# Kernel optimization log

Hardware: AMD Instinct MI355X
Metric: run time of the kernel (lower is better)

## Reference

```python
import jax, jax.numpy as jnp
import numpy as np

B, LQ, LK = 1, 2048, 2048
D, H, KVH, DH = 4096, 32, 8, 128
G = H // KVH  # head groups


def setup_inputs() -> dict:
    key = jax.random.key(0)
    ks = jax.random.split(key, 7)
    s = 0.02
    hidden_q = jax.random.normal(ks[0], (B, LQ, D), dtype=jnp.float32)
    hidden_kv = jax.random.normal(ks[1], (B, LK, D), dtype=jnp.float32)
    # causal boolean mask (batch, len_q, len_k)
    attention_mask = jnp.broadcast_to(jnp.tril(jnp.ones((LQ, LK), dtype=bool)), (B, LQ, LK))
    position_bias = jax.random.normal(ks[2], (H, LQ, LK), dtype=jnp.float32) * 0.1
    Wq = jax.random.normal(ks[3], (D, H * DH), dtype=jnp.float32) * s
    Wk = jax.random.normal(ks[4], (D, KVH * DH), dtype=jnp.float32) * s
    Wv = jax.random.normal(ks[5], (D, KVH * DH), dtype=jnp.float32) * s
    Wo = jax.random.normal(ks[6], (H * DH, D), dtype=jnp.float32) * s
    return {"hidden_q": hidden_q, "hidden_kv": hidden_kv,
            "attention_mask": attention_mask, "position_bias": position_bias,
            "Wq": Wq, "Wk": Wk, "Wv": Wv, "Wo": Wo}


def reference(hidden_q, hidden_kv, attention_mask, position_bias, Wq, Wk, Wv, Wo):
    inv4 = DH ** -0.25  # q and k each scaled by dim_head**-1/4
    q = (hidden_q @ Wq) * inv4            # [B, LQ, H*DH]
    k = (hidden_kv @ Wk) * inv4           # [B, LK, KVH*DH]
    v = hidden_kv @ Wv                     # [B, LK, KVH*DH]
    q = q.reshape(B, LQ, KVH, G, DH)       # group heads for GQA
    k = k.reshape(B, LK, KVH, DH)
    v = v.reshape(B, LK, KVH, DH)
    # score: [B, KVH, G, LQ, LK] -> [B, H, LQ, LK]
    score = jnp.einsum('bqkgd,blkd->bkgql', q, k).reshape(B, H, LQ, LK)
    score = score + position_bias[None]
    mask = attention_mask[:, None]         # [B, 1, LQ, LK]
    score = jnp.where(mask, score, -jnp.inf)
    p = jax.nn.softmax(score, axis=-1)
    p = jnp.where(mask, p, 0.0)
    out = jnp.einsum('bkgql,blkd->bqkgd', p.reshape(B, KVH, G, LQ, LK), v)
    out = out.reshape(B, LQ, H * DH) @ Wo  # [B, LQ, D]
    return out
```

## Files before the change

### kernel.cpp

```cpp
#include <hip/hip_runtime.h>
#include <hip/hip_bf16.h>
#include <cstdint>
#include <cstddef>

typedef __attribute__((ext_vector_type(4))) float f32x4;
typedef __attribute__((ext_vector_type(4))) short s16x4;
typedef __attribute__((ext_vector_type(8))) short s16x8;

#define SLQ 2048
#define SLK 2048
#define SNH 32
#define SDH 128

__device__ __forceinline__ short f2bf(float x) {
  unsigned u = __builtin_bit_cast(unsigned, x);
  u += 0x7FFF + ((u >> 16) & 1);
  return (short)(u >> 16);
}

__device__ __forceinline__ void gload_lds16(const void* g, const void* l) {
  __builtin_amdgcn_global_load_lds((const __attribute__((address_space(1))) void*)g,
                                   (__attribute__((address_space(3))) void*)l,
                                   16, 0, 0);
}

template<int CTRL>
__device__ __forceinline__ float dpp_f32(float x) {
  return __builtin_bit_cast(float, __builtin_amdgcn_update_dpp(
      0, __builtin_bit_cast(int, x), CTRL, 0xF, 0xF, true));
}
__device__ __forceinline__ float rowmax16(float x) {
  x = fmaxf(x, dpp_f32<0x128>(x));
  x = fmaxf(x, dpp_f32<0x124>(x));
  x = fmaxf(x, dpp_f32<0x122>(x));
  x = fmaxf(x, dpp_f32<0x121>(x));
  return x;
}
__device__ __forceinline__ float rowsum16(float x) {
  x += dpp_f32<0x128>(x);
  x += dpp_f32<0x124>(x);
  x += dpp_f32<0x122>(x);
  x += dpp_f32<0x121>(x);
  return x;
}

__global__ void convert_bf16_2(const float* __restrict__ in0, short* __restrict__ out0,
                               const float* __restrict__ in1, short* __restrict__ out1) {
  const int i = blockIdx.x * 256 + threadIdx.x;
  const float* in = blockIdx.y ? in1 : in0;
  short* out = blockIdx.y ? out1 : out0;
  f32x4 a = ((const f32x4*)in)[i];
  s16x4 b;
  b[0] = f2bf(a[0]); b[1] = f2bf(a[1]); b[2] = f2bf(a[2]); b[3] = f2bf(a[3]);
  ((s16x4*)out)[i] = b;
}

__global__ void transpose_all(const float* __restrict__ Wq, const float* __restrict__ Wo,
                              const float* __restrict__ Wk, const float* __restrict__ Wv,
                              short* __restrict__ WqT, short* __restrict__ WoT,
                              short* __restrict__ WkT, short* __restrict__ WvT) {
  __shared__ short T[64][68];
  const int K = 4096;
  int bx = blockIdx.x;
  const float* W; short* Wt; int N;
  if (bx < 64)       { W = Wq; Wt = WqT; N = 4096; }
  else if (bx < 128) { W = Wo; Wt = WoT; N = 4096; bx -= 64; }
  else if (bx < 144) { W = Wk; Wt = WkT; N = 1024; bx -= 128; }
  else               { W = Wv; Wt = WvT; N = 1024; bx -= 144; }
  const int tid = threadIdx.x;
  const int k0 = blockIdx.y * 64, n0 = bx * 64;
  const int r = tid >> 4;
  const int c4 = (tid & 15) * 4;
#pragma unroll
  for (int i = 0; i < 4; ++i) {
    f32x4 a = *(const f32x4*)(W + (size_t)(k0 + r + i * 16) * N + n0 + c4);
#pragma unroll
    for (int j = 0; j < 4; ++j) T[c4 + j][r + i * 16] = f2bf(a[j]);
  }
  __syncthreads();
  const int rn = tid >> 3;
  const int c8 = (tid & 7) * 8;
#pragma unroll
  for (int i = 0; i < 2; ++i) {
    s16x4 v0 = *(const s16x4*)&T[rn + i * 32][c8];
    s16x4 v1 = *(const s16x4*)&T[rn + i * 32][c8 + 4];
    short* dst = Wt + (size_t)(n0 + rn + i * 32) * K + k0 + c8;
    *(s16x4*)dst = v0;
    *(s16x4*)(dst + 4) = v1;
  }
}

template<int CM>
__global__ __launch_bounds__(512, 1)
void gemm_big(const short* __restrict__ A, const short* __restrict__ Bt,
              void* __restrict__ Cv, float scale) {
  __shared__ short As[3][128 * 64];
  __shared__ short Bs[3][256 * 64];
  const int N = 4096, K = 4096;
  const int tid = threadIdx.x, lane = tid & 63, w = tid >> 6;
  const int l15 = lane & 15, lg = lane >> 4;
  const int wr = w >> 2, wc = w & 3;
  const int nbx = N >> 8;
  const int nwg = gridDim.x, b = blockIdx.x;
  const int wg = (b & 7) * (nwg >> 3) + (b >> 3);
  const int m0 = (wg / nbx) * 128, n0 = (wg % nbx) * 256;

  f32x4 acc[4][4];
#pragma unroll
  for (int a = 0; a < 4; ++a)
#pragma unroll
    for (int c = 0; c < 4; ++c)
      acc[a][c] = (f32x4){0.f, 0.f, 0.f, 0.f};

#define GSTAGE(T, BUF) do {                                                    \
    _Pragma("unroll") for (int i_ = 0; i_ < 2; ++i_) {                         \
      const int ci = i_ * 512 + tid, r_ = ci >> 3, c_ = ci & 7;                \
      gload_lds16(A + (size_t)(m0 + r_) * K + (T) * 64 + ((c_ ^ (r_ & 7)) * 8),\
                  (const short*)As[BUF] + ci * 8); }                           \
    _Pragma("unroll") for (int i_ = 0; i_ < 4; ++i_) {                         \
      const int ci = i_ * 512 + tid, r_ = ci >> 3, c_ = ci & 7;                \
      gload_lds16(Bt + (size_t)(n0 + r_) * K + (T) * 64 + ((c_ ^ (r_ & 7)) * 8),\
                  (const short*)Bs[BUF] + ci * 8); }                           \
  } while (0)

  const int NT = K >> 6;
  GSTAGE(0, 0); GSTAGE(1, 1); GSTAGE(2, 2);
  int buf = 0;
  for (int t = 0; t < NT; ++t) {
    if (t + 2 < NT)      asm volatile("s_waitcnt vmcnt(12)" ::: "memory");
    else if (t + 1 < NT) asm volatile("s_waitcnt vmcnt(6)" ::: "memory");
    else                 asm volatile("s_waitcnt vmcnt(0)" ::: "memory");
    __builtin_amdgcn_s_barrier();
    const short* Ab = As[buf];
    const short* Bb = Bs[buf];
    s16x8 af[2][4], bfv[2][4];
#pragma unroll
    for (int kk = 0; kk < 2; ++kk) {
#pragma unroll
      for (int mi = 0; mi < 4; ++mi) {
        const int r = wr * 64 + mi * 16 + l15;
        const int c = (kk * 4 + lg) ^ (r & 7);
        af[kk][mi] = *(const s16x8*)(Ab + (r * 8 + c) * 8);
      }
#pragma unroll
      for (int ni = 0; ni < 4; ++ni) {
        const int r = wc * 64 + ni * 16 + l15;
        const int c = (kk * 4 + lg) ^ (r & 7);
        bfv[kk][ni] = *(const s16x8*)(Bb + (r * 8 + c) * 8);
      }
    }
    __builtin_amdgcn_s_setprio(1);
#pragma unroll
    for (int kk = 0; kk < 2; ++kk)
#pragma unroll
      for (int mi = 0; mi < 4; ++mi)
#pragma unroll
        for (int ni = 0; ni < 4; ++ni)
          acc[mi][ni] = __builtin_amdgcn_mfma_f32_16x16x32_bf16(af[kk][mi], bfv[kk][ni], acc[mi][ni], 0, 0, 0);
    __builtin_amdgcn_s_setprio(0);
    __builtin_amdgcn_s_barrier();
    if (t + 3 < NT) GSTAGE(t + 3, buf);
    buf = (buf == 2) ? 0 : buf + 1;
  }
#undef GSTAGE
#pragma unroll
  for (int mi = 0; mi < 4; ++mi) {
#pragma unroll
    for (int ni = 0; ni < 4; ++ni) {
#pragma unroll
      for (int j = 0; j < 4; ++j) {
        const int rg = m0 + wr * 64 + mi * 16 + lg * 4 + j;
        const int cg = n0 + wc * 64 + ni * 16 + l15;
        const float vv = acc[mi][ni][j] * scale;
        if (CM == 0) ((short*)Cv)[(size_t)rg * N + cg] = f2bf(vv);
        else         ((float*)Cv)[(size_t)rg * N + cg] = vv;
      }
    }
  }
}

__global__ __launch_bounds__(256, 2)
void gemm_kv(const short* __restrict__ A, const short* __restrict__ Bt,
             short* __restrict__ kout, short* __restrict__ vTout, float inv4) {
  __shared__ short As[128][32];
  __shared__ short Bs[128][32];
  const int N = 2048, K = 4096;
  const int tid = threadIdx.x, lane = tid & 63, wid = tid >> 6;
  const int l15 = lane & 15, lg = lane >> 4;
  const int nbx = N >> 7;
  const int nwg = gridDim.x, b = blockIdx.x;
  const int wg = (b & 7) * (nwg >> 3) + (b >> 3);
  const int m0 = (wg / nbx) * 128, n0 = (wg % nbx) * 128;
  const int wm = (wid >> 1) * 64, wn = (wid & 1) * 64;

  f32x4 acc[4][4];
#pragma unroll
  for (int a = 0; a < 4; ++a)
#pragma unroll
    for (int c = 0; c < 4; ++c)
      acc[a][c] = (f32x4){0.f, 0.f, 0.f, 0.f};

  for (int k0 = 0; k0 < K; k0 += 32) {
#pragma unroll
    for (int i = 0; i < 2; ++i) {
      const int c = i * 256 + wid * 64 + lane;
      const int rr = c >> 2, hh = (c & 3) * 8;
      gload_lds16(A  + (size_t)(m0 + rr) * K + k0 + hh,
                  (const short*)As + (size_t)(i * 256 + wid * 64) * 8);
      gload_lds16(Bt + (size_t)(n0 + rr) * K + k0 + hh,
                  (const short*)Bs + (size_t)(i * 256 + wid * 64) * 8);
    }
    __syncthreads();
    s16x8 af[4], bf[4];
#pragma unroll
    for (int mi = 0; mi < 4; ++mi)
      af[mi] = *(const s16x8*)&As[wm + mi * 16 + l15][lg * 8];
#pragma unroll
    for (int ni = 0; ni < 4; ++ni)
      bf[ni] = *(const s16x8*)&Bs[wn + ni * 16 + l15][lg * 8];
#pragma unroll
    for (int mi = 0; mi < 4; ++mi)
#pragma unroll
      for (int ni = 0; ni < 4; ++ni)
        acc[mi][ni] = __builtin_amdgcn_mfma_f32_16x16x32_bf16(af[mi], bf[ni], acc[mi][ni], 0, 0, 0);
    __syncthreads();
  }
  if (n0 < 1024) {
#pragma unroll
    for (int mi = 0; mi < 4; ++mi)
#pragma unroll
      for (int ni = 0; ni < 4; ++ni)
#pragma unroll
        for (int j = 0; j < 4; ++j) {
          const int rg = m0 + wm + mi * 16 + lg * 4 + j;
          const int cg = n0 + wn + ni * 16 + l15;
          kout[(size_t)rg * 1024 + cg] = f2bf(acc[mi][ni][j] * inv4);
        }
  } else {
#pragma unroll
    for (int mi = 0; mi < 4; ++mi)
#pragma unroll
      for (int ni = 0; ni < 4; ++ni) {
        s16x4 wv;
#pragma unroll
        for (int j = 0; j < 4; ++j) wv[j] = f2bf(acc[mi][ni][j]);
        const int rg0 = m0 + wm + mi * 16 + lg * 4;
        const int cg = n0 + wn + ni * 16 + l15 - 1024;
        *(s16x4*)(vTout + (size_t)cg * 2048 + rg0) = wv;
      }
  }
}

__global__ __launch_bounds__(256, 2)
void attn_kernel(const short* __restrict__ q, const short* __restrict__ k,
                 const short* __restrict__ vT, const float* __restrict__ bias,
                 short* __restrict__ o) {
  __shared__ __align__(16) short Ks[64 * 128];
  __shared__ __align__(16) short Vs[2][128 * 64];
  __shared__ __align__(16) float Bb[64 * 64];
  __shared__ __align__(16) short Ps[4][16][72];
  const int tid = threadIdx.x, lane = tid & 63, w = tid >> 6;
  const int l15 = lane & 15, lg = lane >> 4;
  const int b = blockIdx.x;
  const int h = b & 31;
  const int qt = 31 - (b >> 5);
  const int kvh = h >> 2;
  const int nt = qt + 1;

#define STAGE_K(IT) do { const int kv0_ = (IT) * 64;                          \
    _Pragma("unroll") for (int i_ = 0; i_ < 4; ++i_) {                        \
      const int ci = i_ * 256 + tid, r_ = ci >> 4, c_ = ci & 15;              \
      gload_lds16(k + (size_t)(kv0_ + r_) * 1024 + kvh * 128 + ((c_ ^ (r_ & 7)) * 8), \
                  (const short*)Ks + ci * 8); } } while (0)

#define STAGE_V(IT, P) do { const int kv0_ = (IT) * 64;                       \
    _Pragma("unroll") for (int i_ = 0; i_ < 4; ++i_) {                        \
      const int ci = i_ * 256 + tid, r_ = ci >> 3, c_ = ci & 7;               \
      gload_lds16(vT + (size_t)(kvh * 128 + r_) * 2048 + kv0_ + ((c_ ^ (r_ & 7)) * 8), \
                  (const short*)Vs[P] + ci * 8); } } while (0)

#define STAGE_B(IT) do { const int kv0_ = (IT) * 64;                          \
    _Pragma("unroll") for (int i_ = 0; i_ < 4; ++i_) {                        \
      const int ci = i_ * 256 + tid, r_ = ci >> 4, c_ = ci & 15;              \
      gload_lds16(bias + ((size_t)h * SLQ + qt * 64 + r_) * SLK + kv0_ + ((c_ ^ (r_ & 7)) * 4), \
                  (const float*)Bb + ci * 4); } } while (0)

  const int qrow0 = qt * 64 + w * 16 + lg * 4;

  s16x8 qf[4];
  {
    const short* qp = q + (size_t)(qt * 64 + w * 16 + l15) * (SNH * SDH) + h * SDH + lg * 8;
#pragma unroll
    for (int kk = 0; kk < 4; ++kk) qf[kk] = *(const s16x8*)(qp + kk * 32);
  }
  float mrow[4], lrow[4];
  f32x4 oacc[8];
#pragma unroll
  for (int j = 0; j < 4; ++j) { mrow[j] = -1e30f; lrow[j] = 0.f; }
#pragma unroll
  for (int nd = 0; nd < 8; ++nd) oacc[nd] = (f32x4){0.f, 0.f, 0.f, 0.f};

  STAGE_V(0, 0);
  STAGE_K(0);
  STAGE_B(0);

  for (int it = 0; it < nt; ++it) {
    const int p = it & 1;
    const int kv0 = it * 64;
    asm volatile("s_waitcnt vmcnt(4)" ::: "memory");
    __builtin_amdgcn_s_barrier();
    if (it + 1 < nt) STAGE_V(it + 1, p ^ 1);
    f32x4 s[4];
    __builtin_amdgcn_s_setprio(1);
#pragma unroll
    for (int ni = 0; ni < 4; ++ni) {
      s[ni] = (f32x4){0.f, 0.f, 0.f, 0.f};
      const int r = ni * 16 + l15;
#pragma unroll
      for (int kk = 0; kk < 4; ++kk) {
        const int cc = kk * 4 + lg;
        s16x8 kf = *(const s16x8*)(Ks + (r * 16 + (cc ^ (r & 7))) * 8);
        s[ni] = __builtin_amdgcn_mfma_f32_16x16x32_bf16(qf[kk], kf, s[ni], 0, 0, 0);
      }
    }
    __builtin_amdgcn_s_setprio(0);
    if (it + 1 < nt) asm volatile("s_waitcnt vmcnt(4)" ::: "memory");
    else             asm volatile("s_waitcnt vmcnt(0)" ::: "memory");
#pragma unroll
    for (int ni = 0; ni < 4; ++ni) {
#pragma unroll
      for (int j = 0; j < 4; ++j) {
        const int rr = w * 16 + lg * 4 + j;
        const int ch = (ni * 4 + (l15 >> 2)) ^ (rr & 7);
        float sv = s[ni][j] + Bb[rr * 64 + ch * 4 + (l15 & 3)];
        if (it == qt && kv0 + ni * 16 + l15 > qrow0 + j) sv = -1e30f;
        s[ni][j] = sv;
      }
    }
    float pmax[4];
#pragma unroll
    for (int j = 0; j < 4; ++j) {
      float mx = fmaxf(fmaxf(s[0][j], s[1][j]), fmaxf(s[2][j], s[3][j]));
      pmax[j] = rowmax16(mx);
    }
    bool need = (pmax[0] > mrow[0] + 8.f) | (pmax[1] > mrow[1] + 8.f) |
                (pmax[2] > mrow[2] + 8.f) | (pmax[3] > mrow[3] + 8.f);
    if (__any(need)) {
#pragma unroll
      for (int j = 0; j < 4; ++j) {
        const float mn = fmaxf(mrow[j], pmax[j]);
        const float fsj = __expf(mrow[j] - mn);
        mrow[j] = mn;
        lrow[j] *= fsj;
#pragma unroll
        for (int nd = 0; nd < 8; ++nd) oacc[nd][j] *= fsj;
      }
    }
    float ps[4] = {0.f, 0.f, 0.f, 0.f};
#pragma unroll
    for (int ni = 0; ni < 4; ++ni)
#pragma unroll
      for (int j = 0; j < 4; ++j) {
        const float pv = __expf(s[ni][j] - mrow[j]);
        s[ni][j] = pv;
        ps[j] += pv;
      }
#pragma unroll
    for (int j = 0; j < 4; ++j) lrow[j] += rowsum16(ps[j]);
    __builtin_amdgcn_s_barrier();
    if (it + 1 < nt) { STAGE_K(it + 1); STAGE_B(it + 1); }
#pragma unroll
    for (int ni = 0; ni < 4; ++ni)
#pragma unroll
      for (int j = 0; j < 4; ++j)
        Ps[w][lg * 4 + j][ni * 16 + l15] = f2bf(s[ni][j]);
    __builtin_amdgcn_s_setprio(1);
#pragma unroll
    for (int kk2 = 0; kk2 < 2; ++kk2) {
      s16x8 pa = *(const s16x8*)&Ps[w][l15][kk2 * 32 + lg * 8];
#pragma unroll
      for (int nd = 0; nd < 8; ++nd) {
        const int r = nd * 16 + l15;
        const int cc = kk2 * 4 + lg;
        s16x8 vf = *(const s16x8*)(Vs[p] + (r * 8 + (cc ^ (r & 7))) * 8);
        oacc[nd] = __builtin_amdgcn_mfma_f32_16x16x32_bf16(pa, vf, oacc[nd], 0, 0, 0);
      }
    }
    __builtin_amdgcn_s_setprio(0);
  }
#undef STAGE_K
#undef STAGE_V
#undef STAGE_B
#pragma unroll
  for (int j = 0; j < 4; ++j) {
    const float inv = 1.f / lrow[j];
    short* op = o + (size_t)(qrow0 + j) * (SNH * SDH) + h * SDH + l15;
#pragma unroll
    for (int nd = 0; nd < 8; ++nd)
      op[nd * 16] = f2bf(oacc[nd][j] * inv);
  }
}

extern "C" void kernel_launch(void* const* d_in, const int* in_sizes, int n_in,
                              void* d_out, int out_size, void* d_ws, size_t ws_size,
                              hipStream_t stream) {
  (void)in_sizes; (void)n_in; (void)out_size; (void)ws_size;
  const float* hq   = (const float*)d_in[0];
  const float* hkv  = (const float*)d_in[1];
  const float* bias = (const float*)d_in[3];
  const float* Wq   = (const float*)d_in[4];
  const float* Wk   = (const float*)d_in[5];
  const float* Wv   = (const float*)d_in[6];
  const float* Wo   = (const float*)d_in[7];

  short* ws = (short*)d_ws;
  const size_t MEG = 1048576;
  short* hqb  = ws;
  short* hkvb = ws + 8 * MEG;
  short* WT   = ws + 16 * MEG;
  short* WoT  = ws + 32 * MEG;
  short* WkvT = ws + 48 * MEG;
  short* qb   = ws + 56 * MEG;
  short* kb   = ws + 64 * MEG;
  short* vbT  = ws + 66 * MEG;
  short* ob   = hqb;

  const float inv4 = 0.29730177875068026f;

  convert_bf16_2<<<dim3(8192, 2), 256, 0, stream>>>(hq, hqb, hkv, hkvb);
  transpose_all<<<dim3(160, 64), 256, 0, stream>>>(
      Wq, Wo, Wk, Wv, WT, WoT, WkvT, WkvT + (size_t)1024 * 4096);

  gemm_big<0><<<256, 512, 0, stream>>>(hqb, WT, qb, inv4);
  gemm_kv<<<256, 256, 0, stream>>>(hkvb, WkvT, kb, vbT, inv4);

  attn_kernel<<<1024, 256, 0, stream>>>(qb, kb, vbT, bias, ob);

  gemm_big<1><<<256, 512, 0, stream>>>(ob, WoT, (float*)d_out, 1.0f);
}
```

Measured before the change: 462.2 us.

## Load position bias directly into registers and remap GEMM block tiling

The attention kernel no longer stages the position bias tile through LDS. Each lane now loads its 16 bias values straight from global memory into registers one iteration ahead, and the vmcnt waits are adjusted to match. This removes a 16KB LDS buffer and its strided reads, which could improve occupancy, but the per-lane global loads are less coalesced and the waitcnt accounting becomes more fragile. Separately, the big GEMM's block-to-tile mapping is changed to a fixed XCD-aware layout in which each group of eight blocks shares adjacent N tiles.

After: 468.2 us. Within noise of the previous version (+1.3%).

```diff
diff --git a/kernel.cpp b/kernel.cpp
--- a/kernel.cpp
+++ b/kernel.cpp
@@ -100,10 +100,10 @@
   const int tid = threadIdx.x, lane = tid & 63, w = tid >> 6;
   const int l15 = lane & 15, lg = lane >> 4;
   const int wr = w >> 2, wc = w & 3;
-  const int nbx = N >> 8;
-  const int nwg = gridDim.x, b = blockIdx.x;
-  const int wg = (b & 7) * (nwg >> 3) + (b >> 3);
-  const int m0 = (wg / nbx) * 128, n0 = (wg % nbx) * 256;
+  const int b = blockIdx.x;
+  const int cp = b & 7, wi = b >> 3;
+  const int m0 = (wi >> 1) * 128;
+  const int n0 = (cp * 2 + (wi & 1)) * 256;
 
   f32x4 acc[4][4];
 #pragma unroll
@@ -257,7 +257,6 @@
                  short* __restrict__ o) {
   __shared__ __align__(16) short Ks[64 * 128];
   __shared__ __align__(16) short Vs[2][128 * 64];
-  __shared__ __align__(16) float Bb[64 * 64];
   __shared__ __align__(16) short Ps[4][16][72];
   const int tid = threadIdx.x, lane = tid & 63, w = tid >> 6;
   const int l15 = lane & 15, lg = lane >> 4;
@@ -279,13 +278,13 @@
       gload_lds16(vT + (size_t)(kvh * 128 + r_) * 2048 + kv0_ + ((c_ ^ (r_ & 7)) * 8), \
                   (const short*)Vs[P] + ci * 8); } } while (0)
 
-#define STAGE_B(IT) do { const int kv0_ = (IT) * 64;                          \
-    _Pragma("unroll") for (int i_ = 0; i_ < 4; ++i_) {                        \
-      const int ci = i_ * 256 + tid, r_ = ci >> 4, c_ = ci & 15;              \
-      gload_lds16(bias + ((size_t)h * SLQ + qt * 64 + r_) * SLK + kv0_ + ((c_ ^ (r_ & 7)) * 4), \
-                  (const float*)Bb + ci * 4); } } while (0)
-
   const int qrow0 = qt * 64 + w * 16 + lg * 4;
+
+  float bb[4][4];
+#define LOAD_BIAS(IT) do { const float* bp_ = bias + ((size_t)h * SLQ + qrow0) * SLK + (IT) * 64 + l15; \
+    _Pragma("unroll") for (int ni_ = 0; ni_ < 4; ++ni_)                       \
+      _Pragma("unroll") for (int j_ = 0; j_ < 4; ++j_)                        \
+        bb[ni_][j_] = bp_[(size_t)j_ * SLK + ni_ * 16]; } while (0)
 
   s16x8 qf[4];
   {
@@ -302,12 +301,12 @@
 
   STAGE_V(0, 0);
   STAGE_K(0);
-  STAGE_B(0);
+  LOAD_BIAS(0);
 
   for (int it = 0; it < nt; ++it) {
     const int p = it & 1;
     const int kv0 = it * 64;
-    asm volatile("s_waitcnt vmcnt(4)" ::: "memory");
+    asm volatile("s_waitcnt vmcnt(16)" ::: "memory");
     __builtin_amdgcn_s_barrier();
     if (it + 1 < nt) STAGE_V(it + 1, p ^ 1);
     f32x4 s[4];
@@ -324,15 +323,11 @@
       }
     }
     __builtin_amdgcn_s_setprio(0);
-    if (it + 1 < nt) asm volatile("s_waitcnt vmcnt(4)" ::: "memory");
-    else             asm volatile("s_waitcnt vmcnt(0)" ::: "memory");
 #pragma unroll
     for (int ni = 0; ni < 4; ++ni) {
 #pragma unroll
       for (int j = 0; j < 4; ++j) {
-        const int rr = w * 16 + lg * 4 + j;
-        const int ch = (ni * 4 + (l15 >> 2)) ^ (rr & 7);
-        float sv = s[ni][j] + Bb[rr * 64 + ch * 4 + (l15 & 3)];
+        float sv = s[ni][j] + bb[ni][j];
         if (it == qt && kv0 + ni * 16 + l15 > qrow0 + j) sv = -1e30f;
         s[ni][j] = sv;
       }
@@ -368,7 +363,7 @@
 #pragma unroll
     for (int j = 0; j < 4; ++j) lrow[j] += rowsum16(ps[j]);
     __builtin_amdgcn_s_barrier();
-    if (it + 1 < nt) { STAGE_K(it + 1); STAGE_B(it + 1); }
+    if (it + 1 < nt) { STAGE_K(it + 1); LOAD_BIAS(it + 1); }
 #pragma unroll
     for (int ni = 0; ni < 4; ++ni)
 #pragma unroll
@@ -390,7 +385,7 @@
   }
 #undef STAGE_K
 #undef STAGE_V
-#undef STAGE_B
+#undef LOAD_BIAS
 #pragma unroll
   for (int j = 0; j < 4; ++j) {
     const float inv = 1.f / lrow[j];
```
